# Kernel tuning notes

Measured on AMD Instinct MI355X. Metric: run time of the kernel, lower is better.

The kernel has to match this reference:

```python
import jax, jax.numpy as jnp
import numpy as np

HID = 4544; NH = 71; NKV = 1; HD = 64  # Falcon-7B MQA geometry (head_dim hardcoded 64 in _split_heads)
B = 1; U = 32; C = 4; S = 2048          # batch, users, kv chunks, chunk length


def rotate_half(x):
    d = x.shape[-1] // 2
    return jnp.concatenate((-x[..., d:], x[..., :d]), axis=-1)


def setup_inputs() -> dict:
    key = jax.random.key(0)
    ks = jax.random.split(key, 7)
    hidden_states = jax.random.normal(ks[0], (B, U, HID), jnp.float32)
    cos = jax.random.uniform(ks[1], (1, U, 1, HD), jnp.float32, -1.0, 1.0)
    sin = jax.random.uniform(ks[2], (1, U, 1, HD), jnp.float32, -1.0, 1.0)
    k_cache = jax.random.normal(ks[3], (C, B, U, S, HD), jnp.float32)
    v_cache = jax.random.normal(ks[4], (C, B, U, S, HD), jnp.float32)
    attn_masks = jnp.zeros((C, B, U, S), jnp.float32)
    w_qkv = jax.random.normal(ks[5], ((NKV * (NH // NKV + 2)) * HD, HID), jnp.float32) * 0.02
    w_dense = jax.random.normal(ks[6], (HID, HID), jnp.float32) * 0.02
    return {"hidden_states": hidden_states, "cos": cos, "sin": sin,
            "k_cache": k_cache, "v_cache": v_cache, "attn_masks": attn_masks,
            "w_qkv": w_qkv, "w_dense": w_dense}


def reference(hidden_states, cos, sin, k_cache, v_cache, attn_masks, w_qkv, w_dense):
    b, u, _ = hidden_states.shape
    # fused QKV projection (Linear without bias: x @ W.T)
    fused = hidden_states @ w_qkv.T                      # [b,u,(NH+2*NKV)*HD]
    qkv = fused.reshape(b, u, NKV, NH // NKV + 2, HD)    # _split_heads view
    q = qkv[:, :, :, :-2].reshape(b, u, NH, HD)          # query heads
    k_cur = qkv[:, :, :, -2].reshape(b, u, NKV, HD)      # shared MQA key head
    v_cur = qkv[:, :, :, -1].reshape(b, u, NKV, HD)      # shared MQA value head
    # rotary embedding (apply_rotary_pos_emb)
    q = q * cos + rotate_half(q) * sin
    k_cur = k_cur * cos + rotate_half(k_cur) * sin
    inv = 1.0 / jnp.sqrt(jnp.float32(HD))
    # flash-decode over cached chunks: scores [c,b,u,n,s]
    scores = jnp.einsum('bund,cbusd->cbuns', q, k_cache) * inv
    scores = scores + attn_masks[:, :, :, None, :]
    m_c = jnp.max(scores, axis=-1, keepdims=True)        # [c,b,u,n,1] local max
    p = jnp.exp(scores - m_c)
    l_c = jnp.sum(p, axis=-1, keepdims=True)             # local row sums
    # current token = length-1 chunk (its local max is itself, local sum is 1)
    s_cur = jnp.einsum('bund,bued->bune', q, k_cur) * inv  # [b,u,n,1]
    g = jnp.maximum(jnp.max(m_c, axis=0), s_cur)           # global max [b,u,n,1]
    factor = jnp.exp(m_c - g[None])                        # per-chunk rescale
    out = jnp.einsum('cbuns,cbusd->bund', factor * p, v_cache)
    cur_w = jnp.exp(s_cur - g)                             # [b,u,n,1]
    out = out + cur_w * v_cur                              # v_cur broadcasts over heads
    scale = jnp.sum(factor * l_c, axis=0) + cur_w
    out = out / scale
    attn = out.reshape(b, u, NH * HD)
    return attn @ w_dense.T
```

## Files before the change

kernel.cpp:

```cpp
#include <hip/hip_runtime.h>
#include <hip/hip_bf16.h>

typedef __bf16 bf16_t;
typedef __bf16 bf16x8 __attribute__((ext_vector_type(8)));
typedef float  f32x4  __attribute__((ext_vector_type(4)));

#define MFMA16(A,B,C) __builtin_amdgcn_mfma_f32_16x16x32_bf16(A,B,C,0,0,0)

constexpr int HIDc = 4544;
constexpr int NHc  = 71;
constexpr int NHPc = 80;
constexpr int HDc  = 64;
constexpr int Uc   = 32;
constexpr int Sc   = 2048;
constexpr int RQ   = 4672;

constexpr size_t OFF_FUSED = 0;
constexpr size_t OFF_QHI   = 598016;
constexpr size_t OFF_QLO   = 925696;
constexpr size_t OFF_KCUR  = 1253376;
constexpr size_t OFF_VCUR  = 1261568;
constexpr size_t OFF_MP    = 1269760;
constexpr size_t OFF_LP    = 1415168;
constexpr size_t OFF_AHI   = 1560576;
constexpr size_t OFF_ALO   = 1851392;
constexpr size_t OFF_OP    = 2142208;

__device__ __forceinline__ bf16x8 ld8f(const float* base, long eidx) {
  const float* p = base + eidx;
  const f32x4 a = *(const f32x4*)p;
  const f32x4 b = *(const f32x4*)(p + 4);
  bf16x8 r;
  r[0]=(bf16_t)a[0]; r[1]=(bf16_t)a[1]; r[2]=(bf16_t)a[2]; r[3]=(bf16_t)a[3];
  r[4]=(bf16_t)b[0]; r[5]=(bf16_t)b[1]; r[6]=(bf16_t)b[2]; r[7]=(bf16_t)b[3];
  return r;
}

__global__ __launch_bounds__(256) void k_zeros(float* fused, float* out) {
  const int i = blockIdx.x*256 + threadIdx.x;
  if (i < Uc*RQ) fused[i] = 0.f;
  else           out[i - Uc*RQ] = 0.f;
}

__global__ __launch_bounds__(256) void k_qkv(
    const float* __restrict__ hidden, const float* __restrict__ wqkv,
    float* __restrict__ fused)
{
  const int h = blockIdx.x, y = blockIdx.y;
  const int t = threadIdx.x;
  const int wave = t >> 6, lane = t & 63;
  const int c = lane & 15, q4 = lane >> 4;
  const int mt = wave & 1, kh = wave >> 1;
  const int ks0 = y*18;
  const int ksn = min(18, 142 - ks0);
  const int h1  = ksn >> 1;
  const int kbeg = ks0 + (kh ? h1 : 0);
  const int kend = ks0 + (kh ? ksn : h1);
  __shared__ float sD[Uc*HDc];

  const long abase = (long)(mt*16 + c)*HIDc + q4*8;
  const long bbase = ((long)h*64 + c)*HIDc + q4*8;
  f32x4 acc[4] = {};
#pragma unroll 3
  for (int ks = kbeg; ks < kend; ++ks) {
    const bf16x8 af = ld8f(hidden, abase + ks*32);
#pragma unroll
    for (int nf = 0; nf < 4; ++nf) {
      const bf16x8 bv = ld8f(wqkv, bbase + (long)nf*16*HIDc + ks*32);
      acc[nf] = MFMA16(af, bv, acc[nf]);
    }
  }
  if (kh == 0) {
#pragma unroll
    for (int r = 0; r < 4; ++r)
#pragma unroll
      for (int nf = 0; nf < 4; ++nf)
        sD[(mt*16 + q4*4 + r)*64 + nf*16 + c] = acc[nf][r];
  }
  __syncthreads();
  if (kh == 1) {
#pragma unroll
    for (int r = 0; r < 4; ++r)
#pragma unroll
      for (int nf = 0; nf < 4; ++nf)
        sD[(mt*16 + q4*4 + r)*64 + nf*16 + c] += acc[nf][r];
  }
  __syncthreads();
  for (int i = t; i < Uc*HDc; i += 256)
    atomicAdd(&fused[(long)(i >> 6)*RQ + h*64 + (i & 63)], sD[i]);
}

__global__ __launch_bounds__(256) void k_rotary(
    const float* __restrict__ fused,
    const float* __restrict__ cosp, const float* __restrict__ sinp,
    bf16_t* __restrict__ qhi, bf16_t* __restrict__ qlo,
    float* __restrict__ kcur, float* __restrict__ vcur)
{
  const int h = blockIdx.x;
  const int t = threadIdx.x;
  __shared__ float sD[Uc*HDc];
  if (h < 73) {
    for (int i = t; i < Uc*HDc; i += 256)
      sD[i] = fused[(long)(i >> 6)*RQ + h*64 + (i & 63)];
    __syncthreads();
  }
  if (h >= NHc) {
    for (int i = t; i < Uc*HDc; i += 256) {
      const long idx = (((long)(i >> 6))*NHPc + h)*HDc + (i & 63);
      qhi[idx] = (bf16_t)0.f;  qlo[idx] = (bf16_t)0.f;
    }
  }
  if (h >= 73) return;
  for (int i = t; i < Uc*HDc; i += 256) {
    const int u = i >> 6, d = i & 63;
    const float x = sD[i];
    const float partner = sD[i ^ 32];
    const float cs = cosp[u*HDc + d];
    const float sn = sinp[u*HDc + d];
    const float rh = (d < 32) ? -partner : partner;
    const float val = x*cs + rh*sn;
    if (h < NHc) {
      const long idx = ((long)u*NHPc + h)*HDc + d;
      const bf16_t hi = (bf16_t)val;
      qhi[idx] = hi;
      qlo[idx] = (bf16_t)(val - (float)hi);
    } else if (h == NHc) {
      kcur[u*HDc + d] = val;
    } else {
      vcur[u*HDc + d] = x;
    }
  }
}

__global__ __launch_bounds__(256, 1) void k_attn(
    const float* __restrict__ kc, const float* __restrict__ vc,
    const float* __restrict__ masks,
    const bf16_t* __restrict__ qhi, const bf16_t* __restrict__ qlo,
    float* __restrict__ Mp, float* __restrict__ Lp, float* __restrict__ Op,
    const int NPB)
{
  __shared__ float sM[4][NHPc], sL[4][NHPc];
  __shared__ float sO[NHPc*HDc];
  const int u  = blockIdx.x;
  const int pb = blockIdx.y;
  const int tid = threadIdx.x;
  const int wave = tid >> 6;
  const int lane = tid & 63;
  const int c    = lane & 15;
  const int q4   = lane >> 4;
  const int pbpc = NPB >> 2;
  const int keys_pb   = 2048 / pbpc;
  const int keys_wave = keys_pb >> 2;
  const int tcnt      = keys_wave >> 5;
  const int chunk = pb / pbpc;
  const int inner = pb - chunk*pbpc;
  const int s_base = inner*keys_pb + wave*keys_wave;
  const long kvbase = ((long)(chunk*Uc + u))*Sc;

  bf16x8 qh[5][2], ql[5][2];
  const bf16_t* qb  = qhi + ((long)u*NHPc + c)*HDc + q4*8;
  const bf16_t* qb2 = qlo + ((long)u*NHPc + c)*HDc + q4*8;
#pragma unroll
  for (int ht = 0; ht < 5; ++ht)
#pragma unroll
    for (int ks = 0; ks < 2; ++ks) {
      qh[ht][ks] = *(const bf16x8*)(qb  + ht*16*HDc + ks*32);
      ql[ht][ks] = *(const bf16x8*)(qb2 + ht*16*HDc + ks*32);
    }

  float m_i[5], l_i[5];
  f32x4 Oa[5][4] = {};
#pragma unroll
  for (int ht = 0; ht < 5; ++ht) { m_i[ht] = -INFINITY; l_i[ht] = 0.f; }

  for (int t = 0; t < tcnt; ++t) {
    const int s0 = s_base + t*32;
    bf16x8 kf[2][2];
#pragma unroll
    for (int mt2 = 0; mt2 < 2; ++mt2)
#pragma unroll
      for (int ks = 0; ks < 2; ++ks)
        kf[mt2][ks] = ld8f(kc, (kvbase + s0 + mt2*16 + c)*HDc + ks*32 + q4*8);

    f32x4 S[2][5];
#pragma unroll
    for (int mt2 = 0; mt2 < 2; ++mt2)
#pragma unroll
      for (int ht = 0; ht < 5; ++ht) {
        f32x4 s = {};
        s = MFMA16(kf[mt2][0], qh[ht][0], s);
        s = MFMA16(kf[mt2][1], qh[ht][1], s);
        s = MFMA16(kf[mt2][0], ql[ht][0], s);
        s = MFMA16(kf[mt2][1], ql[ht][1], s);
        S[mt2][ht] = s;
      }

    float mk[2][4];
#pragma unroll
    for (int mt2 = 0; mt2 < 2; ++mt2)
#pragma unroll
      for (int r = 0; r < 4; ++r)
        mk[mt2][r] = masks[kvbase + s0 + q4*4 + mt2*16 + r];
#pragma unroll
    for (int mt2 = 0; mt2 < 2; ++mt2)
#pragma unroll
      for (int ht = 0; ht < 5; ++ht)
#pragma unroll
        for (int r = 0; r < 4; ++r)
          S[mt2][ht][r] = S[mt2][ht][r]*0.125f + mk[mt2][r];

    float alpha[5];
#pragma unroll
    for (int ht = 0; ht < 5; ++ht) {
      float tm = S[0][ht][0];
#pragma unroll
      for (int mt2 = 0; mt2 < 2; ++mt2)
#pragma unroll
        for (int r = 0; r < 4; ++r) tm = fmaxf(tm, S[mt2][ht][r]);
      tm = fmaxf(tm, __shfl_xor(tm, 16));
      tm = fmaxf(tm, __shfl_xor(tm, 32));
      const float mn = fmaxf(m_i[ht], tm);
      alpha[ht] = __expf(m_i[ht] - mn);
      m_i[ht] = mn;
    }
#pragma unroll
    for (int mt2 = 0; mt2 < 2; ++mt2)
#pragma unroll
      for (int ht = 0; ht < 5; ++ht)
#pragma unroll
        for (int r = 0; r < 4; ++r)
          S[mt2][ht][r] = __expf(S[mt2][ht][r] - m_i[ht]);
#pragma unroll
    for (int ht = 0; ht < 5; ++ht) {
      float rs = 0.f;
#pragma unroll
      for (int mt2 = 0; mt2 < 2; ++mt2)
#pragma unroll
        for (int r = 0; r < 4; ++r) rs += S[mt2][ht][r];
      rs += __shfl_xor(rs, 16);
      rs += __shfl_xor(rs, 32);
      l_i[ht] = l_i[ht]*alpha[ht] + rs;
    }
#pragma unroll
    for (int ht = 0; ht < 5; ++ht)
#pragma unroll
      for (int r = 0; r < 4; ++r) {
        const float ar = __shfl(alpha[ht], q4*4 + r);
#pragma unroll
        for (int dt = 0; dt < 4; ++dt) Oa[ht][dt][r] *= ar;
      }
    bf16x8 ph[5], pl[5];
#pragma unroll
    for (int ht = 0; ht < 5; ++ht) {
      union { bf16_t e[8]; bf16x8 v; } uh, ul;
#pragma unroll
      for (int j = 0; j < 8; ++j) {
        const int src = (((2*q4 + (j>>2)) & 3) << 4) + c;
        const float v0 = __shfl(S[0][ht][j & 3], src);
        const float v1 = __shfl(S[1][ht][j & 3], src);
        const float val = (q4 < 2) ? v0 : v1;
        const bf16_t hi = (bf16_t)val;
        uh.e[j] = hi;
        ul.e[j] = (bf16_t)(val - (float)hi);
      }
      ph[ht] = uh.v;  pl[ht] = ul.v;
    }
    bf16x8 vf[4];
#pragma unroll
    for (int dt = 0; dt < 4; ++dt) {
      union { bf16_t e[8]; bf16x8 v; } uv;
#pragma unroll
      for (int j = 0; j < 8; ++j)
        uv.e[j] = (bf16_t)vc[(kvbase + s0 + q4*8 + j)*HDc + dt*16 + c];
      vf[dt] = uv.v;
    }
#pragma unroll
    for (int ht = 0; ht < 5; ++ht)
#pragma unroll
      for (int dt = 0; dt < 4; ++dt) {
        Oa[ht][dt] = MFMA16(ph[ht], vf[dt], Oa[ht][dt]);
        Oa[ht][dt] = MFMA16(pl[ht], vf[dt], Oa[ht][dt]);
      }
  }

  if (lane < 16)
#pragma unroll
    for (int ht = 0; ht < 5; ++ht) {
      sM[wave][ht*16 + lane] = m_i[ht];
      sL[wave][ht*16 + lane] = l_i[ht];
    }
  __syncthreads();
#pragma unroll
  for (int ht = 0; ht < 5; ++ht)
#pragma unroll
    for (int r = 0; r < 4; ++r) {
      const int hh = ht*16 + q4*4 + r;
      float mg = fmaxf(fmaxf(sM[0][hh], sM[1][hh]), fmaxf(sM[2][hh], sM[3][hh]));
      mg = fmaxf(mg, -1e30f);
      const float aw = __expf(sM[wave][hh] - mg);
#pragma unroll
      for (int dt = 0; dt < 4; ++dt) Oa[ht][dt][r] *= aw;
    }
  for (int w = 0; w < 4; ++w) {
    if (wave == w) {
#pragma unroll
      for (int ht = 0; ht < 5; ++ht)
#pragma unroll
        for (int dt = 0; dt < 4; ++dt)
#pragma unroll
          for (int r = 0; r < 4; ++r) {
            const int idx = (ht*16 + q4*4 + r)*HDc + dt*16 + c;
            if (w == 0) sO[idx] = Oa[ht][dt][r];
            else        sO[idx] += Oa[ht][dt][r];
          }
    }
    __syncthreads();
  }
  float* op = Op + ((long)u*NPB + pb)*NHc*HDc;
  for (int i = tid; i < NHc*HDc; i += 256) op[i] = sO[i];
  if (wave == 0 && lane < 16) {
#pragma unroll
    for (int ht = 0; ht < 5; ++ht) {
      const int hh = ht*16 + lane;
      if (hh < NHc) {
        float mg = fmaxf(fmaxf(sM[0][hh], sM[1][hh]), fmaxf(sM[2][hh], sM[3][hh]));
        mg = fmaxf(mg, -1e30f);
        float L = 0.f;
#pragma unroll
        for (int w = 0; w < 4; ++w) L += __expf(sM[w][hh] - mg)*sL[w][hh];
        Mp[((long)u*NPB + pb)*NHc + hh] = mg;
        Lp[((long)u*NPB + pb)*NHc + hh] = L;
      }
    }
  }
}

__global__ __launch_bounds__(64) void k_combine(
    const float* __restrict__ Mp, const float* __restrict__ Lp,
    const float* __restrict__ Op,
    const bf16_t* __restrict__ qhi, const bf16_t* __restrict__ qlo,
    const float* __restrict__ kcur, const float* __restrict__ vcur,
    bf16_t* __restrict__ ahi, bf16_t* __restrict__ alo, const int NPB)
{
  const int h = blockIdx.x, u = blockIdx.y;
  const int lane = threadIdx.x;
  const long qidx = ((long)u*NHPc + h)*HDc + lane;
  float pr = ((float)qhi[qidx] + (float)qlo[qidx]) * kcur[u*HDc + lane];
#pragma unroll
  for (int o = 32; o > 0; o >>= 1) pr += __shfl_xor(pr, o);
  const float s_cur = pr * 0.125f;

  float g = s_cur;
  for (int p = 0; p < NPB; ++p)
    g = fmaxf(g, Mp[((long)u*NPB + p)*NHc + h]);
  g = fmaxf(g, -1e30f);
  float sw = 0.f, acc = 0.f;
  const float* ob = Op + (long)u*NPB*NHc*HDc + (long)h*HDc + lane;
  for (int p = 0; p < NPB; ++p) {
    const float f = __expf(Mp[((long)u*NPB + p)*NHc + h] - g);
    sw += f*Lp[((long)u*NPB + p)*NHc + h];
    acc += f*ob[(long)p*NHc*HDc];
  }
  const float cw = __expf(s_cur - g);
  acc += cw * vcur[u*HDc + lane];
  const float attn = acc / (sw + cw);
  const bf16_t hi = (bf16_t)attn;
  ahi[(long)u*HIDc + h*HDc + lane] = hi;
  alo[(long)u*HIDc + h*HDc + lane] = (bf16_t)(attn - (float)hi);
}

__global__ __launch_bounds__(256) void k_outgemm(
    const bf16_t* __restrict__ ahi, const bf16_t* __restrict__ alo,
    const float* __restrict__ wd, float* __restrict__ out)
{
  const int nb = blockIdx.x, y = blockIdx.y;
  const int t = threadIdx.x;
  const int wave = t >> 6, lane = t & 63;
  const int c = lane & 15, q4 = lane >> 4;
  const int mt = wave & 1, kh = wave >> 1;
  const int ks0 = y*18;
  const int ksn = min(18, 142 - ks0);
  const int h1  = ksn >> 1;
  const int kbeg = ks0 + (kh ? h1 : 0);
  const int kend = ks0 + (kh ? ksn : h1);
  __shared__ float sC[Uc*32];

  const bf16_t* aph = ahi + ((long)(mt*16 + c))*HIDc + q4*8;
  const bf16_t* apl = alo + ((long)(mt*16 + c))*HIDc + q4*8;
  const long bbase = ((long)nb*32 + c)*HIDc + q4*8;

  f32x4 acc[2] = {};
#pragma unroll 3
  for (int ks = kbeg; ks < kend; ++ks) {
    const bf16x8 Ah = *(const bf16x8*)(aph + ks*32);
    const bf16x8 Al = *(const bf16x8*)(apl + ks*32);
#pragma unroll
    for (int nf = 0; nf < 2; ++nf) {
      const bf16x8 B = ld8f(wd, bbase + (long)nf*16*HIDc + ks*32);
      acc[nf] = MFMA16(Ah, B, acc[nf]);
      acc[nf] = MFMA16(Al, B, acc[nf]);
    }
  }
  if (kh == 0) {
#pragma unroll
    for (int r = 0; r < 4; ++r)
#pragma unroll
      for (int nf = 0; nf < 2; ++nf)
        sC[(mt*16 + q4*4 + r)*32 + nf*16 + c] = acc[nf][r];
  }
  __syncthreads();
  if (kh == 1) {
#pragma unroll
    for (int r = 0; r < 4; ++r)
#pragma unroll
      for (int nf = 0; nf < 2; ++nf)
        sC[(mt*16 + q4*4 + r)*32 + nf*16 + c] += acc[nf][r];
  }
  __syncthreads();
  for (int i = t; i < Uc*32; i += 256)
    atomicAdd(&out[(long)(i >> 5)*HIDc + nb*32 + (i & 31)], sC[i]);
}

extern "C" void kernel_launch(void* const* d_in, const int* in_sizes, int n_in,
                              void* d_out, int out_size, void* d_ws, size_t ws_size,
                              hipStream_t stream)
{
  const float* hidden = (const float*)d_in[0];
  const float* cosp   = (const float*)d_in[1];
  const float* sinp   = (const float*)d_in[2];
  const float* kcache = (const float*)d_in[3];
  const float* vcache = (const float*)d_in[4];
  const float* masks  = (const float*)d_in[5];
  const float* wqkv   = (const float*)d_in[6];
  const float* wdense = (const float*)d_in[7];
  float* out = (float*)d_out;

  const size_t opb = (size_t)Uc*NHc*HDc*4;
  int NPB = 16;
  if      (ws_size >= OFF_OP + 16*opb) NPB = 16;
  else if (ws_size >= OFF_OP +  8*opb) NPB = 8;
  else if (ws_size >= OFF_OP +  4*opb) NPB = 4;
  else return;

  char* ws = (char*)d_ws;
  float*  fused = (float*)(ws + OFF_FUSED);
  bf16_t* qhi   = (bf16_t*)(ws + OFF_QHI);
  bf16_t* qlo   = (bf16_t*)(ws + OFF_QLO);
  float*  kcur  = (float*)(ws + OFF_KCUR);
  float*  vcur  = (float*)(ws + OFF_VCUR);
  float*  Mp    = (float*)(ws + OFF_MP);
  float*  Lp    = (float*)(ws + OFF_LP);
  bf16_t* ahi   = (bf16_t*)(ws + OFF_AHI);
  bf16_t* alo   = (bf16_t*)(ws + OFF_ALO);
  float*  Op    = (float*)(ws + OFF_OP);

  k_zeros  <<<1152, 256, 0, stream>>>(fused, out);
  k_qkv    <<<dim3(73, 8), 256, 0, stream>>>(hidden, wqkv, fused);
  k_rotary <<<80, 256, 0, stream>>>(fused, cosp, sinp, qhi, qlo, kcur, vcur);
  k_attn   <<<dim3(32, NPB), 256, 0, stream>>>(kcache, vcache, masks, qhi, qlo, Mp, Lp, Op, NPB);
  k_combine<<<dim3(71, 32), 64, 0, stream>>>(Mp, Lp, Op, qhi, qlo, kcur, vcur, ahi, alo, NPB);
  k_outgemm<<<dim3(142, 8), 256, 0, stream>>>(ahi, alo, wdense, out);
}
```

Before: 360.3 us.

## Double-buffer K/V tiles into LDS via async global_load_lds in attention

Each wave in the attention kernel now prefetches its next 32-key K and V tile into a private, XOR-swizzled LDS double buffer using global_load_lds. It waits on vmcnt before computing on the current tile, so HBM loads overlap with the MFMA work. Masks are staged into LDS once up front. The K row mapping is permuted so the P fragments can be built from registers without cross-lane shuffles. This uses about 140KB of dynamic LDS, which limits occupancy to one block per CU. Correctness depends on the swizzle, the row permutation and the hand-written waitcnt values all being right.

New measurement: 353.7 us. Within noise of the previous version (-1.8%).

```diff
diff --git a/kernel.cpp b/kernel.cpp
--- a/kernel.cpp
+++ b/kernel.cpp
@@ -34,6 +34,15 @@
   r[0]=(bf16_t)a[0]; r[1]=(bf16_t)a[1]; r[2]=(bf16_t)a[2]; r[3]=(bf16_t)a[3];
   r[4]=(bf16_t)b[0]; r[5]=(bf16_t)b[1]; r[6]=(bf16_t)b[2]; r[7]=(bf16_t)b[3];
   return r;
+}
+
+__device__ __forceinline__ void cp16(const float* g, float* l) {
+  __builtin_amdgcn_global_load_lds((const __attribute__((address_space(1))) void*)g,
+                                   (__attribute__((address_space(3))) void*)l, 16, 0, 0);
+}
+__device__ __forceinline__ void cp4(const float* g, float* l) {
+  __builtin_amdgcn_global_load_lds((const __attribute__((address_space(1))) void*)g,
+                                   (__attribute__((address_space(3))) void*)l, 4, 0, 0);
 }
 
 __global__ __launch_bounds__(256) void k_zeros(float* fused, float* out) {
@@ -132,6 +141,9 @@
   }
 }
 
+constexpr int ATTN_SMEM_FLOATS = 35456;
+constexpr int ATTN_SMEM_BYTES  = ATTN_SMEM_FLOATS * 4;
+
 __global__ __launch_bounds__(256, 1) void k_attn(
     const float* __restrict__ kc, const float* __restrict__ vc,
     const float* __restrict__ masks,
@@ -139,12 +151,11 @@
     float* __restrict__ Mp, float* __restrict__ Lp, float* __restrict__ Op,
     const int NPB)
 {
-  __shared__ float sM[4][NHPc], sL[4][NHPc];
-  __shared__ float sO[NHPc*HDc];
+  extern __shared__ float smem[];
   const int u  = blockIdx.x;
   const int pb = blockIdx.y;
   const int tid = threadIdx.x;
-  const int wave = tid >> 6;
+  const int wave = __builtin_amdgcn_readfirstlane(tid >> 6);
   const int lane = tid & 63;
   const int c    = lane & 15;
   const int q4   = lane >> 4;
@@ -157,6 +168,33 @@
   const int s_base = inner*keys_pb + wave*keys_wave;
   const long kvbase = ((long)(chunk*Uc + u))*Sc;
 
+  float* const wstage = smem + wave*8192;
+  float* const mwave  = smem + 32768 + wave*512;
+  float* const sM     = smem + 34816;
+  float* const sL     = smem + 35136;
+  float* const sO     = smem;
+
+  const int srow = lane >> 4;
+  const int scol = (lane & 15) << 2;
+
+  {
+    const long tb = (kvbase + s_base) * 64;
+    const float* gK = kc + tb;
+    const float* gV = vc + tb;
+#pragma unroll
+    for (int i = 0; i < 8; ++i) {
+      const int row = i*4 + srow;
+      const int fz = ((row & 7) << 2) ^ (((row >> 3) & 1) << 4);
+      const int off = row*64 + (scol ^ fz);
+      cp16(gK + off, wstage + i*256);
+      cp16(gV + off, wstage + 2048 + i*256);
+    }
+    const int nmc = keys_wave >> 6;
+    const float* gM = masks + kvbase + s_base;
+    for (int i = 0; i < nmc; ++i)
+      cp4(gM + i*64 + lane, mwave + i*64);
+  }
+
   bf16x8 qh[5][2], ql[5][2];
   const bf16_t* qb  = qhi + ((long)u*NHPc + c)*HDc + q4*8;
   const bf16_t* qb2 = qlo + ((long)u*NHPc + c)*HDc + q4*8;
@@ -173,14 +211,61 @@
 #pragma unroll
   for (int ht = 0; ht < 5; ++ht) { m_i[ht] = -INFINITY; l_i[ht] = 0.f; }
 
+  const int krow0 = ((c >> 2) << 3) + (c & 3);
+
   for (int t = 0; t < tcnt; ++t) {
-    const int s0 = s_base + t*32;
+    float* const lK = wstage + (t & 1)*4096;
+    float* const lV = lK + 2048;
+
+    if (t + 1 < tcnt) {
+      float* const nK = wstage + ((t+1) & 1)*4096;
+      const long tb = (kvbase + s_base + (long)(t+1)*32) * 64;
+      const float* gK = kc + tb;
+      const float* gV = vc + tb;
+#pragma unroll
+      for (int i = 0; i < 8; ++i) {
+        const int row = i*4 + srow;
+        const int fz = ((row & 7) << 2) ^ (((row >> 3) & 1) << 4);
+        const int off = row*64 + (scol ^ fz);
+        cp16(gK + off, nK + i*256);
+        cp16(gV + off, nK + 2048 + i*256);
+      }
+      asm volatile("s_waitcnt vmcnt(16)" ::: "memory");
+    } else {
+      asm volatile("s_waitcnt vmcnt(0)" ::: "memory");
+    }
+    __builtin_amdgcn_sched_barrier(0);
+
     bf16x8 kf[2][2];
 #pragma unroll
-    for (int mt2 = 0; mt2 < 2; ++mt2)
-#pragma unroll
-      for (int ks = 0; ks < 2; ++ks)
-        kf[mt2][ks] = ld8f(kc, (kvbase + s0 + mt2*16 + c)*HDc + ks*32 + q4*8);
+    for (int mt2 = 0; mt2 < 2; ++mt2) {
+      const int row = krow0 + mt2*4;
+      const int fz = ((row & 7) << 2) ^ (((row >> 3) & 1) << 4);
+#pragma unroll
+      for (int ks = 0; ks < 2; ++ks) {
+        const int b0 = row*64 + ((ks*32 + q4*8) ^ fz);
+        const int b1 = row*64 + ((ks*32 + q4*8 + 4) ^ fz);
+        const f32x4 a = *(const f32x4*)(lK + b0);
+        const f32x4 b = *(const f32x4*)(lK + b1);
+        bf16x8 r;
+        r[0]=(bf16_t)a[0]; r[1]=(bf16_t)a[1]; r[2]=(bf16_t)a[2]; r[3]=(bf16_t)a[3];
+        r[4]=(bf16_t)b[0]; r[5]=(bf16_t)b[1]; r[6]=(bf16_t)b[2]; r[7]=(bf16_t)b[3];
+        kf[mt2][ks] = r;
+      }
+    }
+
+    bf16x8 vf[4];
+#pragma unroll
+    for (int dt = 0; dt < 4; ++dt) {
+      union { bf16_t e[8]; bf16x8 v; } uv;
+#pragma unroll
+      for (int j = 0; j < 8; ++j) {
+        const int row = q4*8 + j;
+        const int fz = ((row & 7) << 2) ^ (((row >> 3) & 1) << 4);
+        uv.e[j] = (bf16_t)lV[row*64 + ((dt*16 + c) ^ fz)];
+      }
+      vf[dt] = uv.v;
+    }
 
     f32x4 S[2][5];
 #pragma unroll
@@ -200,7 +285,7 @@
     for (int mt2 = 0; mt2 < 2; ++mt2)
 #pragma unroll
       for (int r = 0; r < 4; ++r)
-        mk[mt2][r] = masks[kvbase + s0 + q4*4 + mt2*16 + r];
+        mk[mt2][r] = mwave[t*32 + q4*8 + mt2*4 + r];
 #pragma unroll
     for (int mt2 = 0; mt2 < 2; ++mt2)
 #pragma unroll
@@ -255,25 +340,13 @@
       union { bf16_t e[8]; bf16x8 v; } uh, ul;
 #pragma unroll
       for (int j = 0; j < 8; ++j) {
-        const int src = (((2*q4 + (j>>2)) & 3) << 4) + c;
-        const float v0 = __shfl(S[0][ht][j & 3], src);
-        const float v1 = __shfl(S[1][ht][j & 3], src);
-        const float val = (q4 < 2) ? v0 : v1;
+        const float val = (j < 4) ? S[0][ht][j] : S[1][ht][j & 3];
         const bf16_t hi = (bf16_t)val;
         uh.e[j] = hi;
         ul.e[j] = (bf16_t)(val - (float)hi);
       }
       ph[ht] = uh.v;  pl[ht] = ul.v;
     }
-    bf16x8 vf[4];
-#pragma unroll
-    for (int dt = 0; dt < 4; ++dt) {
-      union { bf16_t e[8]; bf16x8 v; } uv;
-#pragma unroll
-      for (int j = 0; j < 8; ++j)
-        uv.e[j] = (bf16_t)vc[(kvbase + s0 + q4*8 + j)*HDc + dt*16 + c];
-      vf[dt] = uv.v;
-    }
 #pragma unroll
     for (int ht = 0; ht < 5; ++ht)
 #pragma unroll
@@ -286,8 +359,8 @@
   if (lane < 16)
 #pragma unroll
     for (int ht = 0; ht < 5; ++ht) {
-      sM[wave][ht*16 + lane] = m_i[ht];
-      sL[wave][ht*16 + lane] = l_i[ht];
+      sM[wave*80 + ht*16 + lane] = m_i[ht];
+      sL[wave*80 + ht*16 + lane] = l_i[ht];
     }
   __syncthreads();
 #pragma unroll
@@ -295,9 +368,9 @@
 #pragma unroll
     for (int r = 0; r < 4; ++r) {
       const int hh = ht*16 + q4*4 + r;
-      float mg = fmaxf(fmaxf(sM[0][hh], sM[1][hh]), fmaxf(sM[2][hh], sM[3][hh]));
+      float mg = fmaxf(fmaxf(sM[hh], sM[80 + hh]), fmaxf(sM[160 + hh], sM[240 + hh]));
       mg = fmaxf(mg, -1e30f);
-      const float aw = __expf(sM[wave][hh] - mg);
+      const float aw = __expf(sM[wave*80 + hh] - mg);
 #pragma unroll
       for (int dt = 0; dt < 4; ++dt) Oa[ht][dt][r] *= aw;
     }
@@ -323,11 +396,11 @@
     for (int ht = 0; ht < 5; ++ht) {
       const int hh = ht*16 + lane;
       if (hh < NHc) {
-        float mg = fmaxf(fmaxf(sM[0][hh], sM[1][hh]), fmaxf(sM[2][hh], sM[3][hh]));
+        float mg = fmaxf(fmaxf(sM[hh], sM[80 + hh]), fmaxf(sM[160 + hh], sM[240 + hh]));
         mg = fmaxf(mg, -1e30f);
         float L = 0.f;
 #pragma unroll
-        for (int w = 0; w < 4; ++w) L += __expf(sM[w][hh] - mg)*sL[w][hh];
+        for (int w = 0; w < 4; ++w) L += __expf(sM[w*80 + hh] - mg)*sL[w*80 + hh];
         Mp[((long)u*NPB + pb)*NHc + hh] = mg;
         Lp[((long)u*NPB + pb)*NHc + hh] = L;
       }
@@ -454,10 +527,13 @@
   bf16_t* alo   = (bf16_t*)(ws + OFF_ALO);
   float*  Op    = (float*)(ws + OFF_OP);
 
+  hipFuncSetAttribute(reinterpret_cast<const void*>(k_attn),
+                      hipFuncAttributeMaxDynamicSharedMemorySize, ATTN_SMEM_BYTES);
+
   k_zeros  <<<1152, 256, 0, stream>>>(fused, out);
   k_qkv    <<<dim3(73, 8), 256, 0, stream>>>(hidden, wqkv, fused);
   k_rotary <<<80, 256, 0, stream>>>(fused, cosp, sinp, qhi, qlo, kcur, vcur);
-  k_attn   <<<dim3(32, NPB), 256, 0, stream>>>(kcache, vcache, masks, qhi, qlo, Mp, Lp, Op, NPB);
+  k_attn   <<<dim3(32, NPB), 256, ATTN_SMEM_BYTES, stream>>>(kcache, vcache, masks, qhi, qlo, Mp, Lp, Op, NPB);
   k_combine<<<dim3(71, 32), 64, 0, stream>>>(Mp, Lp, Op, qhi, qlo, kcur, vcur, ahi, alo, NPB);
   k_outgemm<<<dim3(142, 8), 256, 0, stream>>>(ahi, alo, wdense, out);
 }
```
